# Performance work log

Hardware: AMD Instinct MI355X
Metric: run time of the kernel (lower is better)

## Reference

```python
import jax, jax.numpy as jnp
import numpy as np

D = 128
EPS = 1e-6


def setup_inputs() -> dict:
    key = jax.random.key(0)
    k1, k2, k3, k4 = jax.random.split(key, 4)
    N, NQ, NK = 32, 2048, 2048
    queries = jax.random.normal(k1, (N, NQ, D), dtype=jnp.float32)
    keys = jax.random.normal(k2, (N, NK, D), dtype=jnp.float32)
    values = jax.random.normal(k3, (N, NK, D), dtype=jnp.float32)
    # multiplicative (soft) mask in [0,1)
    mask = jax.random.uniform(k4, (N, NQ, NK), dtype=jnp.float32)
    return {"queries": queries, "keys": keys, "values": values, "mask": mask}


def reference(queries, keys, values, mask):
    # scaled dot-product scores: N x n_q x n_k
    scaled = jnp.einsum("bqd,bkd->bqk", queries, keys) / jnp.sqrt(jnp.float32(D))
    attn = jax.nn.softmax(scaled, axis=2)
    # post-softmax multiplicative masking + renormalization
    attn = attn * mask
    attn = attn / (jnp.sum(attn, axis=2, keepdims=True) + EPS)
    return jnp.einsum("bqk,bkd->bqd", attn, values)
```

## Files before the change

kernel.cpp:

```cpp
#include <hip/hip_runtime.h>

#define NB   32
#define NQL  2048
#define NKL  2048
#define DH   128
#define QBLK 64
#define KBLK 64
#define NT   (NKL / KBLK)
#define EPS  1e-6f

typedef __bf16 bf16x8 __attribute__((ext_vector_type(8)));
typedef __bf16 bf16x4 __attribute__((ext_vector_type(4)));
typedef float  f32x4  __attribute__((ext_vector_type(4)));

__global__ __launch_bounds__(256) void
prep_kv(const float* __restrict__ Kg, const float* __restrict__ Vg,
        unsigned short* __restrict__ Kimg, unsigned short* __restrict__ Vimg)
{
    __shared__ float T[64 * 132];
    const int t = threadIdx.x;
    if (blockIdx.x < NB * NT) {
        const int blk = blockIdx.x;
        const int rK  = t >> 2;
        const int x0  = (t & 3) * 32;
        const int swz = (rK & 7) << 3;
        const float* src = Kg + ((size_t)blk * 64 + rK) * DH;
        unsigned short* dst = Kimg + ((size_t)blk << 13) + rK * 128;
        #pragma unroll
        for (int i = 0; i < 4; ++i) {
            const int c0 = (x0 + i * 8) ^ swz;
            float4 a = *(const float4*)(src + c0);
            float4 c = *(const float4*)(src + c0 + 4);
            *(bf16x8*)(dst + x0 + i * 8) =
                (bf16x8){ (__bf16)a.x, (__bf16)a.y, (__bf16)a.z, (__bf16)a.w,
                          (__bf16)c.x, (__bf16)c.y, (__bf16)c.z, (__bf16)c.w };
        }
    } else {
        const int blk = blockIdx.x - NB * NT;
        {
            const int r  = t >> 2;
            const int c0 = (t & 3) * 32;
            const float* src = Vg + ((size_t)blk * 64 + r) * DH + c0;
            #pragma unroll
            for (int j = 0; j < 8; ++j)
                *(float4*)&T[r * 132 + c0 + j * 4] = *(const float4*)(src + j * 4);
        }
        __syncthreads();
        {
            const int dV  = t >> 1;
            const int yh  = (t & 1) * 32;
            const int swz = (dV & 7) << 3;
            unsigned short* dst = Vimg + ((size_t)blk << 13) + dV * 64 + yh;
            #pragma unroll
            for (int i = 0; i < 4; ++i) {
                const int ks = (yh + i * 8) ^ swz;
                bf16x8 o;
                #pragma unroll
                for (int j = 0; j < 8; ++j) o[j] = (__bf16)T[(ks + j) * 132 + dV];
                *(bf16x8*)(dst + i * 8) = o;
            }
        }
    }
}


#define LOAD_IMG(KT) do { \
    const char* ks_ = KimgB + (((size_t)(b * 32 + (KT))) << 14) + woff + lby; \
    const char* vs_ = VimgB + (((size_t)(b * 32 + (KT))) << 14) + woff + lby; \
    ik0 = *(const bf16x8*)(ks_ +    0);  ik1 = *(const bf16x8*)(ks_ + 1024); \
    ik2 = *(const bf16x8*)(ks_ + 2048);  ik3 = *(const bf16x8*)(ks_ + 3072); \
    iv0 = *(const bf16x8*)(vs_ +    0);  iv1 = *(const bf16x8*)(vs_ + 1024); \
    iv2 = *(const bf16x8*)(vs_ + 2048);  iv3 = *(const bf16x8*)(vs_ + 3072); \
} while (0)

#define STW_IMG(KB, VB) do { \
    char* kd_ = (char*)(KB) + woff + lby; \
    char* vd_ = (char*)(VB) + woff + lby; \
    *(bf16x8*)(kd_ +    0) = ik0;  *(bf16x8*)(kd_ + 1024) = ik1; \
    *(bf16x8*)(kd_ + 2048) = ik2;  *(bf16x8*)(kd_ + 3072) = ik3; \
    *(bf16x8*)(vd_ +    0) = iv0;  *(bf16x8*)(vd_ + 1024) = iv1; \
    *(bf16x8*)(vd_ + 2048) = iv2;  *(bf16x8*)(vd_ + 3072) = iv3; \
} while (0)

#define LOAD_M(K0, R0, R1, R2, R3) do { \
    const float* mb_ = mbase + (K0) + lg * 4; \
    R0 = *(const float4*)(mb_ +  0);  R1 = *(const float4*)(mb_ + 16); \
    R2 = *(const float4*)(mb_ + 32);  R3 = *(const float4*)(mb_ + 48); \
} while (0)

#define COMPUTE(KB, VB, M0, M1, M2, M3) do { \
    f32x4 sacc[4]; \
    _Pragma("unroll") for (int m = 0; m < 4; ++m) sacc[m] = (f32x4){0.f,0.f,0.f,0.f}; \
    __builtin_amdgcn_s_setprio(1); \
    _Pragma("unroll") for (int m = 0; m < 4; ++m) { \
        _Pragma("unroll") for (int c = 0; c < 4; ++c) { \
            bf16x8 af = *(bf16x8*)&KB[(m * 16 + lq) * 128 + ((c * 32 + lg * 8) ^ swzL)]; \
            sacc[m] = __builtin_amdgcn_mfma_f32_16x16x32_bf16(af, qf[c], sacc[m], 0, 0, 0); \
        } \
    } \
    __builtin_amdgcn_s_setprio(0); \
    float mk_[16] = { M0.x, M0.y, M0.z, M0.w,  M1.x, M1.y, M1.z, M1.w, \
                      M2.x, M2.y, M2.z, M2.w,  M3.x, M3.y, M3.z, M3.w }; \
    float sv[4][4], tmax = -1e30f; \
    _Pragma("unroll") for (int m = 0; m < 4; ++m) \
        _Pragma("unroll") for (int r = 0; r < 4; ++r) { \
            sv[m][r] = sacc[m][r] * scale; \
            tmax = fmaxf(tmax, sv[m][r]); \
        } \
    tmax = fmaxf(tmax, __shfl_xor(tmax, 16)); \
    tmax = fmaxf(tmax, __shfl_xor(tmax, 32)); \
    if (!__all(tmax - m_run <= 8.f)) { \
        const float mnew  = fmaxf(m_run, tmax); \
        const float alpha = __expf(m_run - mnew); \
        m_run = mnew;  z_part *= alpha;  s_part *= alpha; \
        float alr[4]; \
        _Pragma("unroll") for (int r = 0; r < 4; ++r) alr[r] = __shfl(alpha, lg * 4 + r); \
        _Pragma("unroll") for (int n = 0; n < 8; ++n) \
            _Pragma("unroll") for (int r = 0; r < 4; ++r) oacc[n][r] *= alr[r]; \
    } \
    float zl = 0.f, sl = 0.f, pm[4][4]; \
    _Pragma("unroll") for (int m = 0; m < 4; ++m) \
        _Pragma("unroll") for (int r = 0; r < 4; ++r) { \
            float p = __expf(sv[m][r] - m_run); \
            zl += p; \
            float pq = p * mk_[m * 4 + r]; \
            sl += pq;  pm[m][r] = pq; \
        } \
    z_part += zl;  s_part += sl; \
    _Pragma("unroll") for (int m = 0; m < 4; ++m) \
        *(bf16x4*)&Ps[w][lq][m * 16 + lg * 4] = \
            (bf16x4){ (__bf16)pm[m][0], (__bf16)pm[m][1], (__bf16)pm[m][2], (__bf16)pm[m][3] }; \
    __builtin_amdgcn_s_setprio(1); \
    _Pragma("unroll") for (int kc = 0; kc < 2; ++kc) { \
        bf16x8 pa = *(bf16x8*)&Ps[w][lq][kc * 32 + lg * 8]; \
        _Pragma("unroll") for (int n = 0; n < 8; ++n) { \
            bf16x8 vv = *(bf16x8*)&VB[(n * 16 + lq) * 64 + ((kc * 32 + lg * 8) ^ swzL)]; \
            oacc[n] = __builtin_amdgcn_mfma_f32_16x16x32_bf16(pa, vv, oacc[n], 0, 0, 0); \
        } \
    } \
    __builtin_amdgcn_s_setprio(0); \
} while (0)

#define SOFT_BARRIER() do { \
    asm volatile("s_waitcnt lgkmcnt(0)" ::: "memory"); \
    __builtin_amdgcn_sched_barrier(0); \
    __builtin_amdgcn_s_barrier(); \
    __builtin_amdgcn_sched_barrier(0); \
} while (0)

#define ITER(KT, KBc, VBc, KBn, VBn, MU0,MU1,MU2,MU3, ML0,ML1,ML2,ML3) do { \
    if ((KT) + 1 < NT) STW_IMG(KBn, VBn); \
    if ((KT) + 2 < NT) LOAD_IMG((KT) + 2); \
    if ((KT) + 1 < NT) LOAD_M(((KT) + 1) * KBLK, ML0, ML1, ML2, ML3); \
    COMPUTE(KBc, VBc, MU0, MU1, MU2, MU3); \
    if ((KT) + 1 < NT) SOFT_BARRIER(); \
} while (0)

__global__ __launch_bounds__(256, 2) void
attn_main(const float* __restrict__ Qg, const unsigned short* __restrict__ Kimg,
          const unsigned short* __restrict__ Vimg, const float* __restrict__ Mg,
          float* __restrict__ Og)
{
    const int wg = ((blockIdx.x & 7) << 7) | (blockIdx.x >> 3);
    const int b  = wg >> 5;
    const int q0 = (wg & 31) * QBLK;

    const int t  = threadIdx.x;
    const int w  = t >> 6;
    const int l  = t & 63;
    const int lq = l & 15;
    const int lg = l >> 4;
    const int swzL = (lq & 7) << 3;
    const int woff = w * 4096;
    const int lby  = l * 16;

    __shared__ __align__(16) unsigned short Kb0[64 * 128];
    __shared__ __align__(16) unsigned short Kb1[64 * 128];
    __shared__ __align__(16) unsigned short Vb0[128 * 64];
    __shared__ __align__(16) unsigned short Vb1[128 * 64];
    __shared__ __align__(16) unsigned short Ps[4][16][72];

    const char* KimgB = (const char*)Kimg;
    const char* VimgB = (const char*)Vimg;

    const int qrow = q0 + w * 16 + lq;

    bf16x8 qf[4];
    {
        const float* qb = Qg + ((size_t)b * NQL + qrow) * DH;
        #pragma unroll
        for (int c = 0; c < 4; ++c) {
            const float* p = qb + c * 32 + lg * 8;
            float4 x = *(const float4*)(p);
            float4 y = *(const float4*)(p + 4);
            qf[c] = (bf16x8){ (__bf16)x.x, (__bf16)x.y, (__bf16)x.z, (__bf16)x.w,
                              (__bf16)y.x, (__bf16)y.y, (__bf16)y.z, (__bf16)y.w };
        }
    }

    float m_run = -1e30f, z_part = 0.f, s_part = 0.f;
    f32x4 oacc[8];
    #pragma unroll
    for (int n = 0; n < 8; ++n) oacc[n] = (f32x4){0.f, 0.f, 0.f, 0.f};

    const float* mbase = Mg + ((size_t)b * NQL + qrow) * NKL;
    const float scale = 0.08838834764831845f;

    bf16x8 ik0, ik1, ik2, ik3, iv0, iv1, iv2, iv3;
    float4 mA0, mA1, mA2, mA3, mB0, mB1, mB2, mB3;

    LOAD_IMG(0);
    LOAD_M(0, mA0, mA1, mA2, mA3);
    STW_IMG(Kb0, Vb0);
    LOAD_IMG(1);
    SOFT_BARRIER();

    for (int kt = 0; kt < NT; kt += 2) {
        ITER(kt,     Kb0, Vb0, Kb1, Vb1, mA0,mA1,mA2,mA3, mB0,mB1,mB2,mB3);
        ITER(kt + 1, Kb1, Vb1, Kb0, Vb0, mB0,mB1,mB2,mB3, mA0,mA1,mA2,mA3);
    }

    float z = z_part + __shfl_xor(z_part, 16);
    z += __shfl_xor(z, 32);
    float s = s_part + __shfl_xor(s_part, 16);
    s += __shfl_xor(s, 32);
    const float inv = 1.f / (s + EPS * z);
    float ivr[4];
    #pragma unroll
    for (int r = 0; r < 4; ++r) ivr[r] = __shfl(inv, lg * 4 + r);

    float* ob = Og + ((size_t)b * NQL + q0 + w * 16) * DH;
    #pragma unroll
    for (int n = 0; n < 8; ++n)
        #pragma unroll
        for (int r = 0; r < 4; ++r)
            ob[(size_t)(lg * 4 + r) * DH + n * 16 + lq] = oacc[n][r] * ivr[r];
}

__global__ __launch_bounds__(256, 3) void
attn_fb(const float* __restrict__ Qg, const float* __restrict__ Kg,
        const float* __restrict__ Vg, const float* __restrict__ Mg,
        float* __restrict__ Og)
{
    const int wg = ((blockIdx.x & 7) << 7) | (blockIdx.x >> 3);
    const int b  = wg >> 5;
    const int q0 = (wg & 31) * QBLK;
    const int t  = threadIdx.x;
    const int w  = t >> 6;
    const int l  = t & 63;
    const int lq = l & 15;
    const int lg = l >> 4;
    __shared__ __align__(16) unsigned short Ks[64 * 128];
    __shared__ __align__(16) unsigned short Vs[128 * 64];
    __shared__ __align__(16) unsigned short Ps[4][16][72];
    const int rK   = t >> 2;
    const int cK   = (t & 3) * 32;
    const int dV   = t >> 1;
    const int khV  = t & 1;
    const int swzK = (rK & 7) << 3;
    const int swzV = (dV & 7) << 3;
    const int swzL = (lq & 7) << 3;
    const int qrow = q0 + w * 16 + lq;
    bf16x8 qf[4];
    {
        const float* qb = Qg + ((size_t)b * NQL + qrow) * DH;
        #pragma unroll
        for (int c = 0; c < 4; ++c) {
            const float* p = qb + c * 32 + lg * 8;
            float4 x = *(const float4*)(p);
            float4 y = *(const float4*)(p + 4);
            qf[c] = (bf16x8){ (__bf16)x.x, (__bf16)x.y, (__bf16)x.z, (__bf16)x.w,
                              (__bf16)y.x, (__bf16)y.y, (__bf16)y.z, (__bf16)y.w };
        }
    }
    float m_run = -1e30f, z_part = 0.f, s_part = 0.f;
    f32x4 oacc[8];
    #pragma unroll
    for (int n = 0; n < 8; ++n) oacc[n] = (f32x4){0.f, 0.f, 0.f, 0.f};
    const float* kbase = Kg + (size_t)b * NKL * DH;
    const float* vbase = Vg + (size_t)b * NKL * DH;
    const float* mbase = Mg + ((size_t)b * NQL + qrow) * NKL;
    const float scale = 0.08838834764831845f;
    for (int kt = 0; kt < NT; ++kt) {
        const int k0 = kt * KBLK;
        float mkf[16];
        {
            const float* mb = mbase + k0 + lg * 4;
            #pragma unroll
            for (int m = 0; m < 4; ++m) {
                float4 x = *(const float4*)(mb + m * 16);
                mkf[m*4+0]=x.x; mkf[m*4+1]=x.y; mkf[m*4+2]=x.z; mkf[m*4+3]=x.w;
            }
        }
        __syncthreads();
        {
            const float* kb = kbase + (size_t)(k0 + rK) * DH + cK;
            #pragma unroll
            for (int i = 0; i < 4; ++i) {
                float4 a = *(const float4*)(kb + i * 8);
                float4 c = *(const float4*)(kb + i * 8 + 4);
                *(bf16x8*)&Ks[rK * 128 + ((cK + i * 8) ^ swzK)] =
                    (bf16x8){ (__bf16)a.x, (__bf16)a.y, (__bf16)a.z, (__bf16)a.w,
                              (__bf16)c.x, (__bf16)c.y, (__bf16)c.z, (__bf16)c.w };
            }
            const float* vb = vbase + (size_t)(k0 + khV * 32) * DH + dV;
            #pragma unroll
            for (int i = 0; i < 4; ++i) {
                bf16x8 o;
                #pragma unroll
                for (int j = 0; j < 8; ++j) o[j] = (__bf16)vb[(i * 8 + j) * DH];
                *(bf16x8*)&Vs[dV * 64 + (((khV << 5) + i * 8) ^ swzV)] = o;
            }
        }
        __syncthreads();
        f32x4 sacc[4];
        #pragma unroll
        for (int m = 0; m < 4; ++m) sacc[m] = (f32x4){0.f,0.f,0.f,0.f};
        #pragma unroll
        for (int m = 0; m < 4; ++m)
            #pragma unroll
            for (int c = 0; c < 4; ++c) {
                bf16x8 af = *(bf16x8*)&Ks[(m * 16 + lq) * 128 + ((c * 32 + lg * 8) ^ swzL)];
                sacc[m] = __builtin_amdgcn_mfma_f32_16x16x32_bf16(af, qf[c], sacc[m], 0, 0, 0);
            }
        float sv[4][4], tmax = -1e30f;
        #pragma unroll
        for (int m = 0; m < 4; ++m)
            #pragma unroll
            for (int r = 0; r < 4; ++r) {
                sv[m][r] = sacc[m][r] * scale;
                tmax = fmaxf(tmax, sv[m][r]);
            }
        tmax = fmaxf(tmax, __shfl_xor(tmax, 16));
        tmax = fmaxf(tmax, __shfl_xor(tmax, 32));
        if (!__all(tmax - m_run <= 8.f)) {
            const float mnew  = fmaxf(m_run, tmax);
            const float alpha = __expf(m_run - mnew);
            m_run = mnew; z_part *= alpha; s_part *= alpha;
            float alr[4];
            #pragma unroll
            for (int r = 0; r < 4; ++r) alr[r] = __shfl(alpha, lg * 4 + r);
            #pragma unroll
            for (int n = 0; n < 8; ++n)
                #pragma unroll
                for (int r = 0; r < 4; ++r) oacc[n][r] *= alr[r];
        }
        float zl = 0.f, sl = 0.f, pm[4][4];
        #pragma unroll
        for (int m = 0; m < 4; ++m)
            #pragma unroll
            for (int r = 0; r < 4; ++r) {
                float p = __expf(sv[m][r] - m_run);
                zl += p;
                float pq = p * mkf[m * 4 + r];
                sl += pq; pm[m][r] = pq;
            }
        z_part += zl; s_part += sl;
        #pragma unroll
        for (int m = 0; m < 4; ++m)
            *(bf16x4*)&Ps[w][lq][m * 16 + lg * 4] =
                (bf16x4){ (__bf16)pm[m][0], (__bf16)pm[m][1], (__bf16)pm[m][2], (__bf16)pm[m][3] };
        #pragma unroll
        for (int kc = 0; kc < 2; ++kc) {
            bf16x8 pa = *(bf16x8*)&Ps[w][lq][kc * 32 + lg * 8];
            #pragma unroll
            for (int n = 0; n < 8; ++n) {
                bf16x8 vv = *(bf16x8*)&Vs[(n * 16 + lq) * 64 + ((kc * 32 + lg * 8) ^ swzL)];
                oacc[n] = __builtin_amdgcn_mfma_f32_16x16x32_bf16(pa, vv, oacc[n], 0, 0, 0);
            }
        }
    }
    float z = z_part + __shfl_xor(z_part, 16);
    z += __shfl_xor(z, 32);
    float s = s_part + __shfl_xor(s_part, 16);
    s += __shfl_xor(s, 32);
    const float inv = 1.f / (s + EPS * z);
    float ivr[4];
    #pragma unroll
    for (int r = 0; r < 4; ++r) ivr[r] = __shfl(inv, lg * 4 + r);
    float* ob = Og + ((size_t)b * NQL + q0 + w * 16) * DH;
    #pragma unroll
    for (int n = 0; n < 8; ++n)
        #pragma unroll
        for (int r = 0; r < 4; ++r)
            ob[(size_t)(lg * 4 + r) * DH + n * 16 + lq] = oacc[n][r] * ivr[r];
}

extern "C" void kernel_launch(void* const* d_in, const int* in_sizes, int n_in,
                              void* d_out, int out_size, void* d_ws, size_t ws_size,
                              hipStream_t stream)
{
    (void)in_sizes; (void)n_in; (void)out_size;
    const float* Q = (const float*)d_in[0];
    const float* K = (const float*)d_in[1];
    const float* V = (const float*)d_in[2];
    const float* M = (const float*)d_in[3];
    float* O = (float*)d_out;

    const size_t imgElems = (size_t)NB * NKL * DH;
    const size_t need     = 2 * imgElems * sizeof(unsigned short);

    if (ws_size >= need) {
        unsigned short* Kimg = (unsigned short*)d_ws;
        unsigned short* Vimg = Kimg + imgElems;
        prep_kv<<<dim3(2 * NB * NT), 256, 0, stream>>>(K, V, Kimg, Vimg);
        attn_main<<<dim3(NB * (NQL / QBLK)), 256, 0, stream>>>(Q, Kimg, Vimg, M, O);
    } else {
        attn_fb<<<dim3(NB * (NQL / QBLK)), 256, 0, stream>>>(Q, K, V, M, O);
    }
}
```

Before: 193.7 us.

## Load K/V MFMA fragments directly from global memory in pre-permuted layout

The prep kernel now writes K and V bf16 images in the exact per-lane MFMA fragment order, so the attention kernel can read each fragment with one coalesced 16-byte global load per lane. This removes the LDS double buffering, swizzle, staging stores and per-tile barriers, which frees shared memory and allows the occupancy hint to rise from 2 to 3 blocks per SM. In exchange there is no explicit prefetch or software pipelining, so global/L2 latency for K, V and the mask now falls inside each iteration. Every wave also re-reads the whole K/V tile from cache instead of sharing one LDS copy.

```diff
diff --git a/kernel.cpp b/kernel.cpp
--- a/kernel.cpp
+++ b/kernel.cpp
@@ -22,24 +22,22 @@
     if (blockIdx.x < NB * NT) {
         const int blk = blockIdx.x;
         const int rK  = t >> 2;
-        const int x0  = (t & 3) * 32;
-        const int swz = (rK & 7) << 3;
-        const float* src = Kg + ((size_t)blk * 64 + rK) * DH;
-        unsigned short* dst = Kimg + ((size_t)blk << 13) + rK * 128;
+        const int c   = t & 3;
+        const int m   = rK >> 4, lq = rK & 15;
+        const float* src = Kg + ((size_t)blk * 64 + rK) * DH + c * 32;
+        unsigned short* dst = Kimg + ((size_t)blk << 13);
         #pragma unroll
         for (int i = 0; i < 4; ++i) {
-            const int c0 = (x0 + i * 8) ^ swz;
-            float4 a = *(const float4*)(src + c0);
-            float4 c = *(const float4*)(src + c0 + 4);
-            *(bf16x8*)(dst + x0 + i * 8) =
+            float4 a = *(const float4*)(src + i * 8);
+            float4 d = *(const float4*)(src + i * 8 + 4);
+            *(bf16x8*)(dst + ((size_t)((m * 4 + c) * 64 + i * 16 + lq)) * 8) =
                 (bf16x8){ (__bf16)a.x, (__bf16)a.y, (__bf16)a.z, (__bf16)a.w,
-                          (__bf16)c.x, (__bf16)c.y, (__bf16)c.z, (__bf16)c.w };
+                          (__bf16)d.x, (__bf16)d.y, (__bf16)d.z, (__bf16)d.w };
         }
     } else {
         const int blk = blockIdx.x - NB * NT;
         {
-            const int r  = t >> 2;
-            const int c0 = (t & 3) * 32;
+            const int r = t >> 2, c0 = (t & 3) * 32;
             const float* src = Vg + ((size_t)blk * 64 + r) * DH + c0;
             #pragma unroll
             for (int j = 0; j < 8; ++j)
@@ -47,116 +45,22 @@
         }
         __syncthreads();
         {
-            const int dV  = t >> 1;
-            const int yh  = (t & 1) * 32;
-            const int swz = (dV & 7) << 3;
-            unsigned short* dst = Vimg + ((size_t)blk << 13) + dV * 64 + yh;
+            const int dV = t >> 1, khV = t & 1;
+            const int n = dV >> 4, lq = dV & 15;
+            unsigned short* dst = Vimg + ((size_t)blk << 13);
             #pragma unroll
             for (int i = 0; i < 4; ++i) {
-                const int ks = (yh + i * 8) ^ swz;
                 bf16x8 o;
                 #pragma unroll
-                for (int j = 0; j < 8; ++j) o[j] = (__bf16)T[(ks + j) * 132 + dV];
-                *(bf16x8*)(dst + i * 8) = o;
+                for (int j = 0; j < 8; ++j)
+                    o[j] = (__bf16)T[(khV * 32 + i * 8 + j) * 132 + dV];
+                *(bf16x8*)(dst + ((size_t)((n * 2 + khV) * 64 + i * 16 + lq)) * 8) = o;
             }
         }
     }
 }
 
-
-#define LOAD_IMG(KT) do { \
-    const char* ks_ = KimgB + (((size_t)(b * 32 + (KT))) << 14) + woff + lby; \
-    const char* vs_ = VimgB + (((size_t)(b * 32 + (KT))) << 14) + woff + lby; \
-    ik0 = *(const bf16x8*)(ks_ +    0);  ik1 = *(const bf16x8*)(ks_ + 1024); \
-    ik2 = *(const bf16x8*)(ks_ + 2048);  ik3 = *(const bf16x8*)(ks_ + 3072); \
-    iv0 = *(const bf16x8*)(vs_ +    0);  iv1 = *(const bf16x8*)(vs_ + 1024); \
-    iv2 = *(const bf16x8*)(vs_ + 2048);  iv3 = *(const bf16x8*)(vs_ + 3072); \
-} while (0)
-
-#define STW_IMG(KB, VB) do { \
-    char* kd_ = (char*)(KB) + woff + lby; \
-    char* vd_ = (char*)(VB) + woff + lby; \
-    *(bf16x8*)(kd_ +    0) = ik0;  *(bf16x8*)(kd_ + 1024) = ik1; \
-    *(bf16x8*)(kd_ + 2048) = ik2;  *(bf16x8*)(kd_ + 3072) = ik3; \
-    *(bf16x8*)(vd_ +    0) = iv0;  *(bf16x8*)(vd_ + 1024) = iv1; \
-    *(bf16x8*)(vd_ + 2048) = iv2;  *(bf16x8*)(vd_ + 3072) = iv3; \
-} while (0)
-
-#define LOAD_M(K0, R0, R1, R2, R3) do { \
-    const float* mb_ = mbase + (K0) + lg * 4; \
-    R0 = *(const float4*)(mb_ +  0);  R1 = *(const float4*)(mb_ + 16); \
-    R2 = *(const float4*)(mb_ + 32);  R3 = *(const float4*)(mb_ + 48); \
-} while (0)
-
-#define COMPUTE(KB, VB, M0, M1, M2, M3) do { \
-    f32x4 sacc[4]; \
-    _Pragma("unroll") for (int m = 0; m < 4; ++m) sacc[m] = (f32x4){0.f,0.f,0.f,0.f}; \
-    __builtin_amdgcn_s_setprio(1); \
-    _Pragma("unroll") for (int m = 0; m < 4; ++m) { \
-        _Pragma("unroll") for (int c = 0; c < 4; ++c) { \
-            bf16x8 af = *(bf16x8*)&KB[(m * 16 + lq) * 128 + ((c * 32 + lg * 8) ^ swzL)]; \
-            sacc[m] = __builtin_amdgcn_mfma_f32_16x16x32_bf16(af, qf[c], sacc[m], 0, 0, 0); \
-        } \
-    } \
-    __builtin_amdgcn_s_setprio(0); \
-    float mk_[16] = { M0.x, M0.y, M0.z, M0.w,  M1.x, M1.y, M1.z, M1.w, \
-                      M2.x, M2.y, M2.z, M2.w,  M3.x, M3.y, M3.z, M3.w }; \
-    float sv[4][4], tmax = -1e30f; \
-    _Pragma("unroll") for (int m = 0; m < 4; ++m) \
-        _Pragma("unroll") for (int r = 0; r < 4; ++r) { \
-            sv[m][r] = sacc[m][r] * scale; \
-            tmax = fmaxf(tmax, sv[m][r]); \
-        } \
-    tmax = fmaxf(tmax, __shfl_xor(tmax, 16)); \
-    tmax = fmaxf(tmax, __shfl_xor(tmax, 32)); \
-    if (!__all(tmax - m_run <= 8.f)) { \
-        const float mnew  = fmaxf(m_run, tmax); \
-        const float alpha = __expf(m_run - mnew); \
-        m_run = mnew;  z_part *= alpha;  s_part *= alpha; \
-        float alr[4]; \
-        _Pragma("unroll") for (int r = 0; r < 4; ++r) alr[r] = __shfl(alpha, lg * 4 + r); \
-        _Pragma("unroll") for (int n = 0; n < 8; ++n) \
-            _Pragma("unroll") for (int r = 0; r < 4; ++r) oacc[n][r] *= alr[r]; \
-    } \
-    float zl = 0.f, sl = 0.f, pm[4][4]; \
-    _Pragma("unroll") for (int m = 0; m < 4; ++m) \
-        _Pragma("unroll") for (int r = 0; r < 4; ++r) { \
-            float p = __expf(sv[m][r] - m_run); \
-            zl += p; \
-            float pq = p * mk_[m * 4 + r]; \
-            sl += pq;  pm[m][r] = pq; \
-        } \
-    z_part += zl;  s_part += sl; \
-    _Pragma("unroll") for (int m = 0; m < 4; ++m) \
-        *(bf16x4*)&Ps[w][lq][m * 16 + lg * 4] = \
-            (bf16x4){ (__bf16)pm[m][0], (__bf16)pm[m][1], (__bf16)pm[m][2], (__bf16)pm[m][3] }; \
-    __builtin_amdgcn_s_setprio(1); \
-    _Pragma("unroll") for (int kc = 0; kc < 2; ++kc) { \
-        bf16x8 pa = *(bf16x8*)&Ps[w][lq][kc * 32 + lg * 8]; \
-        _Pragma("unroll") for (int n = 0; n < 8; ++n) { \
-            bf16x8 vv = *(bf16x8*)&VB[(n * 16 + lq) * 64 + ((kc * 32 + lg * 8) ^ swzL)]; \
-            oacc[n] = __builtin_amdgcn_mfma_f32_16x16x32_bf16(pa, vv, oacc[n], 0, 0, 0); \
-        } \
-    } \
-    __builtin_amdgcn_s_setprio(0); \
-} while (0)
-
-#define SOFT_BARRIER() do { \
-    asm volatile("s_waitcnt lgkmcnt(0)" ::: "memory"); \
-    __builtin_amdgcn_sched_barrier(0); \
-    __builtin_amdgcn_s_barrier(); \
-    __builtin_amdgcn_sched_barrier(0); \
-} while (0)
-
-#define ITER(KT, KBc, VBc, KBn, VBn, MU0,MU1,MU2,MU3, ML0,ML1,ML2,ML3) do { \
-    if ((KT) + 1 < NT) STW_IMG(KBn, VBn); \
-    if ((KT) + 2 < NT) LOAD_IMG((KT) + 2); \
-    if ((KT) + 1 < NT) LOAD_M(((KT) + 1) * KBLK, ML0, ML1, ML2, ML3); \
-    COMPUTE(KBc, VBc, MU0, MU1, MU2, MU3); \
-    if ((KT) + 1 < NT) SOFT_BARRIER(); \
-} while (0)
-
-__global__ __launch_bounds__(256, 2) void
+__global__ __launch_bounds__(256, 3) void
 attn_main(const float* __restrict__ Qg, const unsigned short* __restrict__ Kimg,
           const unsigned short* __restrict__ Vimg, const float* __restrict__ Mg,
           float* __restrict__ Og)
@@ -170,18 +74,8 @@
     const int l  = t & 63;
     const int lq = l & 15;
     const int lg = l >> 4;
-    const int swzL = (lq & 7) << 3;
-    const int woff = w * 4096;
-    const int lby  = l * 16;
-
-    __shared__ __align__(16) unsigned short Kb0[64 * 128];
-    __shared__ __align__(16) unsigned short Kb1[64 * 128];
-    __shared__ __align__(16) unsigned short Vb0[128 * 64];
-    __shared__ __align__(16) unsigned short Vb1[128 * 64];
+
     __shared__ __align__(16) unsigned short Ps[4][16][72];
-
-    const char* KimgB = (const char*)Kimg;
-    const char* VimgB = (const char*)Vimg;
 
     const int qrow = q0 + w * 16 + lq;
 
@@ -203,21 +97,93 @@
     #pragma unroll
     for (int n = 0; n < 8; ++n) oacc[n] = (f32x4){0.f, 0.f, 0.f, 0.f};
 
-    const float* mbase = Mg + ((size_t)b * NQL + qrow) * NKL;
+    const char* kbase = (const char*)Kimg + ((size_t)b << 19) + (size_t)l * 16;
+    const char* vbase = (const char*)Vimg + ((size_t)b << 19) + (size_t)l * 16;
+    const float* mbase = Mg + ((size_t)b * NQL + qrow) * NKL + lg * 4;
     const float scale = 0.08838834764831845f;
 
-    bf16x8 ik0, ik1, ik2, ik3, iv0, iv1, iv2, iv3;
-    float4 mA0, mA1, mA2, mA3, mB0, mB1, mB2, mB3;
-
-    LOAD_IMG(0);
-    LOAD_M(0, mA0, mA1, mA2, mA3);
-    STW_IMG(Kb0, Vb0);
-    LOAD_IMG(1);
-    SOFT_BARRIER();
-
-    for (int kt = 0; kt < NT; kt += 2) {
-        ITER(kt,     Kb0, Vb0, Kb1, Vb1, mA0,mA1,mA2,mA3, mB0,mB1,mB2,mB3);
-        ITER(kt + 1, Kb1, Vb1, Kb0, Vb0, mB0,mB1,mB2,mB3, mA0,mA1,mA2,mA3);
+    for (int kt = 0; kt < NT; ++kt) {
+        const char* kt_k = kbase + ((size_t)kt << 14);
+        const char* kt_v = vbase + ((size_t)kt << 14);
+
+        const float* mb = mbase + kt * KBLK;
+        float4 mk0 = *(const float4*)(mb +  0);
+        float4 mk1 = *(const float4*)(mb + 16);
+        float4 mk2 = *(const float4*)(mb + 32);
+        float4 mk3 = *(const float4*)(mb + 48);
+
+        f32x4 sacc[4];
+        #pragma unroll
+        for (int m = 0; m < 4; ++m) sacc[m] = (f32x4){0.f, 0.f, 0.f, 0.f};
+        __builtin_amdgcn_s_setprio(1);
+        #pragma unroll
+        for (int m = 0; m < 4; ++m) {
+            bf16x8 kf0 = *(const bf16x8*)(kt_k + (m * 4 + 0) * 1024);
+            bf16x8 kf1 = *(const bf16x8*)(kt_k + (m * 4 + 1) * 1024);
+            bf16x8 kf2 = *(const bf16x8*)(kt_k + (m * 4 + 2) * 1024);
+            bf16x8 kf3 = *(const bf16x8*)(kt_k + (m * 4 + 3) * 1024);
+            sacc[m] = __builtin_amdgcn_mfma_f32_16x16x32_bf16(kf0, qf[0], sacc[m], 0, 0, 0);
+            sacc[m] = __builtin_amdgcn_mfma_f32_16x16x32_bf16(kf1, qf[1], sacc[m], 0, 0, 0);
+            sacc[m] = __builtin_amdgcn_mfma_f32_16x16x32_bf16(kf2, qf[2], sacc[m], 0, 0, 0);
+            sacc[m] = __builtin_amdgcn_mfma_f32_16x16x32_bf16(kf3, qf[3], sacc[m], 0, 0, 0);
+        }
+        __builtin_amdgcn_s_setprio(0);
+
+        float mk_[16] = { mk0.x, mk0.y, mk0.z, mk0.w,  mk1.x, mk1.y, mk1.z, mk1.w,
+                          mk2.x, mk2.y, mk2.z, mk2.w,  mk3.x, mk3.y, mk3.z, mk3.w };
+        float sv[4][4], tmax = -1e30f;
+        #pragma unroll
+        for (int m = 0; m < 4; ++m)
+            #pragma unroll
+            for (int r = 0; r < 4; ++r) {
+                sv[m][r] = sacc[m][r] * scale;
+                tmax = fmaxf(tmax, sv[m][r]);
+            }
+        tmax = fmaxf(tmax, __shfl_xor(tmax, 16));
+        tmax = fmaxf(tmax, __shfl_xor(tmax, 32));
+
+        if (!__all(tmax - m_run <= 8.f)) {
+            const float mnew  = fmaxf(m_run, tmax);
+            const float alpha = __expf(m_run - mnew);
+            m_run = mnew;  z_part *= alpha;  s_part *= alpha;
+            float alr[4];
+            #pragma unroll
+            for (int r = 0; r < 4; ++r) alr[r] = __shfl(alpha, lg * 4 + r);
+            #pragma unroll
+            for (int n = 0; n < 8; ++n)
+                #pragma unroll
+                for (int r = 0; r < 4; ++r) oacc[n][r] *= alr[r];
+        }
+
+        float zl = 0.f, sl = 0.f, pm[4][4];
+        #pragma unroll
+        for (int m = 0; m < 4; ++m)
+            #pragma unroll
+            for (int r = 0; r < 4; ++r) {
+                float p = __expf(sv[m][r] - m_run);
+                zl += p;
+                float pq = p * mk_[m * 4 + r];
+                sl += pq;  pm[m][r] = pq;
+            }
+        z_part += zl;  s_part += sl;
+
+        #pragma unroll
+        for (int m = 0; m < 4; ++m)
+            *(bf16x4*)&Ps[w][lq][m * 16 + lg * 4] =
+                (bf16x4){ (__bf16)pm[m][0], (__bf16)pm[m][1],
+                          (__bf16)pm[m][2], (__bf16)pm[m][3] };
+
+        __builtin_amdgcn_s_setprio(1);
+        #pragma unroll
+        for (int kc = 0; kc < 2; ++kc) {
+            bf16x8 pa = *(bf16x8*)&Ps[w][lq][kc * 32 + lg * 8];
+            #pragma unroll
+            for (int n = 0; n < 8; ++n) {
+                bf16x8 vv = *(const bf16x8*)(kt_v + (n * 2 + kc) * 1024);
+                oacc[n] = __builtin_amdgcn_mfma_f32_16x16x32_bf16(pa, vv, oacc[n], 0, 0, 0);
+            }
+        }
+        __builtin_amdgcn_s_setprio(0);
     }
 
     float z = z_part + __shfl_xor(z_part, 16);
```

Measured after the change: 312.1 us. 61.1% more time.
